# Performance work log

Hardware: AMD Instinct MI355X
Metric: run time of the kernel (lower is better)

Reference implementation:

```python
import jax, jax.numpy as jnp
import numpy as np


def setup_inputs() -> dict:
    key = jax.random.key(0)
    k1, k2, k3 = jax.random.split(key, 3)
    B, D, T, DEPTH = 16384, 512, 64, 6
    x = jax.random.normal(k1, (B, D), dtype=jnp.float32)
    # per-tree learned params, stacked over the tree axis (num_trees)
    feature_selectors = jax.random.normal(k2, (T, DEPTH, D), dtype=jnp.float32)
    thresholds = jnp.zeros((T, DEPTH), dtype=jnp.float32)
    leaf_weights = jax.random.normal(k3, (T, 2 ** DEPTH, 1), dtype=jnp.float32)
    return {"x": x, "feature_selectors": feature_selectors,
            "thresholds": thresholds, "leaf_weights": leaf_weights}


def reference(x, feature_selectors, thresholds, leaf_weights):
    # x: [B, D]; feature_selectors: [T, depth, D]; thresholds: [T, depth]
    # leaf_weights: [T, 2^depth, 1]
    B = x.shape[0]
    T, depth, _ = feature_selectors.shape
    # all trees' split logits in one GEMM: [B, T, depth]
    logits = jnp.einsum('bi,tdi->btd', x, feature_selectors) - thresholds
    probs = jax.nn.sigmoid(logits)
    # probs_stack[..., 0] = p, probs_stack[..., 1] = 1 - p  -> [B, T, depth, 2]
    probs_stack = jnp.stack([probs, 1.0 - probs], axis=-1)
    # build leaf probabilities via repeated outer products over the depth axis
    leaf = probs_stack[:, :, 0]  # [B, T, 2]
    for d in range(1, depth):
        # [B, T, 2^d, 1] * [B, T, 1, 2] -> [B, T, 2^(d+1)]
        leaf = (leaf[..., :, None] * probs_stack[:, :, d][:, :, None, :]).reshape(B, T, -1)
    # per-tree leaf_probs @ weights, summed over trees -> [B, 1]
    out = jnp.einsum('btl,tlo->bo', leaf, leaf_weights)
    return out
```

## Files before the change

### kernel.cpp

```cpp
#include <hip/hip_runtime.h>


#define DD     512
#define NCOL   384
#define PKELT  (NCOL * DD)
#define XSTR   522
#define PRSTR  388

typedef __bf16 bf16_t;
typedef __bf16 bf16x8 __attribute__((ext_vector_type(8)));
typedef __bf16 bf16x4 __attribute__((ext_vector_type(4)));
typedef float  f32x4  __attribute__((ext_vector_type(4)));

static __device__ __forceinline__ float b2f(unsigned int u16) {
  unsigned int t = u16 << 16;
  float f;
  __builtin_memcpy(&f, &t, 4);
  return f;
}

__global__ __launch_bounds__(256) void node_pack(const float* __restrict__ fsel,
                                                 bf16_t* __restrict__ pk)
{
  int tid  = blockIdx.x * 256 + threadIdx.x;
  int lane = tid & 63;
  int ksg  = (tid >> 6) & 15;
  int cf   = tid >> 10;
  int col  = cf * 16 + (lane & 15);
  int k    = ksg * 32 + (lane >> 4) * 8;
  float4 f0 = *reinterpret_cast<const float4*>(fsel + (size_t)col * DD + k);
  float4 f1 = *reinterpret_cast<const float4*>(fsel + (size_t)col * DD + k + 4);
  bf16x8 v;
  v[0] = (bf16_t)f0.x; v[1] = (bf16_t)f0.y; v[2] = (bf16_t)f0.z; v[3] = (bf16_t)f0.w;
  v[4] = (bf16_t)f1.x; v[5] = (bf16_t)f1.y; v[6] = (bf16_t)f1.z; v[7] = (bf16_t)f1.w;
  #pragma unroll
  for (int c = 0; c < 8; ++c)
    *reinterpret_cast<bf16x8*>(pk + (size_t)c * PKELT + (size_t)tid * 8) = v;
}

__global__ __launch_bounds__(512, 2) void node_fused(
    const float*  __restrict__ x,
    const bf16_t* __restrict__ pk,
    const float*  __restrict__ thr,
    const float*  __restrict__ lw,
    float*        __restrict__ out)
{
  __shared__ bf16_t xs[64 * XSTR];
  __shared__ bf16_t pr[64 * PRSTR];

  const int tid  = threadIdx.x;
  const int lane = tid & 63;
  const int wv   = tid >> 6;
  const int rowblk = blockIdx.x * 64;
  const int c   = lane & 15;
  const int kg  = lane >> 4;

  const float* xr0 = x + (size_t)(rowblk + (tid >> 4)) * DD + ((tid & 15) << 2);
  const float* xr1 = xr0 + (size_t)32 * DD;
  bf16_t* xw0 = &xs[(tid >> 4) * XSTR + ((tid & 15) << 2)];
  bf16_t* xw1 = &xs[((tid >> 4) + 32) * XSTR + ((tid & 15) << 2)];

  float th[3];
  #pragma unroll
  for (int f = 0; f < 3; ++f) th[f] = thr[wv * 48 + f * 16 + c];

  float4 stg[2][2];

  #define ISSUE(n, buf)                                                         \
    do {                                                                        \
      int off_ = (n) * 64;                                                      \
      asm volatile("" : "+v"(off_));                                            \
      stg[buf][0] = *reinterpret_cast<const float4*>(xr0 + off_);               \
      stg[buf][1] = *reinterpret_cast<const float4*>(xr1 + off_);               \
    } while (0)

  #define WRITE(n, buf)                                                         \
    do {                                                                        \
      bf16x4 v0_, v1_;                                                          \
      v0_[0]=(bf16_t)stg[buf][0].x; v0_[1]=(bf16_t)stg[buf][0].y;               \
      v0_[2]=(bf16_t)stg[buf][0].z; v0_[3]=(bf16_t)stg[buf][0].w;               \
      v1_[0]=(bf16_t)stg[buf][1].x; v1_[1]=(bf16_t)stg[buf][1].y;               \
      v1_[2]=(bf16_t)stg[buf][1].z; v1_[3]=(bf16_t)stg[buf][1].w;               \
      *reinterpret_cast<bf16x4*>(xw0 + (n) * 64) = v0_;                         \
      *reinterpret_cast<bf16x4*>(xw1 + (n) * 64) = v1_;                         \
    } while (0)

  #define LOAD_BH(B_, n)                                                        \
    do {                                                                        \
      const bf16_t* q_ = pk + (size_t)(blockIdx.x & 7) * PKELT +                \
                         (size_t)lane * 8 + (size_t)(n) * 1024 +                \
                         (size_t)wv * 3 * 8192;                                 \
      asm volatile("" : "+v"(q_));                                              \
      _Pragma("unroll")                                                         \
      for (int f_ = 0; f_ < 3; ++f_)                                            \
        _Pragma("unroll")                                                       \
        for (int ks_ = 0; ks_ < 2; ++ks_)                                       \
          B_[f_][ks_] = *reinterpret_cast<const bf16x8*>(q_ + f_ * 8192 + ks_ * 512); \
    } while (0)

  bf16x8 bhA[3][2], bhB[3][2];

  ISSUE(0, 0);
  LOAD_BH(bhA, 0);
  LOAD_BH(bhB, 1);
  ISSUE(1, 1);
  WRITE(0, 0);
  ISSUE(2, 0);
  asm volatile("s_waitcnt lgkmcnt(0)" ::: "memory");
  __builtin_amdgcn_s_barrier();

  f32x4 acc[4][3];
  #pragma unroll
  for (int t = 0; t < 4; ++t)
    #pragma unroll
    for (int f = 0; f < 3; ++f) acc[t][f] = (f32x4){0.f, 0.f, 0.f, 0.f};

  #define CHUNK(ch, CUR)                                                        \
    do {                                                                        \
      __builtin_amdgcn_s_setprio(1);                                            \
      _Pragma("unroll")                                                         \
      for (int t = 0; t < 4; ++t) {                                             \
        _Pragma("unroll")                                                       \
        for (int ks = 0; ks < 2; ++ks) {                                        \
          bf16x8 a = *reinterpret_cast<const bf16x8*>(                          \
              &xs[(t * 16 + c) * XSTR + (ch) * 64 + ks * 32 + kg * 8]);         \
          acc[t][0] = __builtin_amdgcn_mfma_f32_16x16x32_bf16(a, CUR[0][ks], acc[t][0], 0, 0, 0); \
          acc[t][1] = __builtin_amdgcn_mfma_f32_16x16x32_bf16(a, CUR[1][ks], acc[t][1], 0, 0, 0); \
          acc[t][2] = __builtin_amdgcn_mfma_f32_16x16x32_bf16(a, CUR[2][ks], acc[t][2], 0, 0, 0); \
        }                                                                       \
      }                                                                         \
      __builtin_amdgcn_s_setprio(0);                                            \
      if ((ch) + 2 < 8) LOAD_BH(CUR, (ch) + 2);                                 \
      if ((ch) < 7) {                                                           \
        WRITE((ch) + 1, ((ch) + 1) & 1);                                        \
        if ((ch) < 5) ISSUE((ch) + 3, ((ch) + 1) & 1);                          \
        asm volatile("s_waitcnt lgkmcnt(0)" ::: "memory");                      \
        __builtin_amdgcn_s_barrier();                                           \
      }                                                                         \
    } while (0)

  CHUNK(0, bhA);
  CHUNK(1, bhB);
  CHUNK(2, bhA);
  CHUNK(3, bhB);
  CHUNK(4, bhA);
  CHUNK(5, bhB);
  CHUNK(6, bhA);
  CHUNK(7, bhB);
  #undef CHUNK
  #undef ISSUE
  #undef WRITE
  #undef LOAD_BH

  #pragma unroll
  for (int t = 0; t < 4; ++t) {
    #pragma unroll
    for (int f = 0; f < 3; ++f) {
      const int col = wv * 48 + f * 16 + c;
      #pragma unroll
      for (int r = 0; r < 4; ++r) {
        const int row = t * 16 + kg * 4 + r;
        float z = acc[t][f][r] - th[f];
        float p = 1.0f / (1.0f + __expf(-z));
        pr[row * PRSTR + col] = (bf16_t)p;
      }
    }
  }
  asm volatile("s_waitcnt lgkmcnt(0)" ::: "memory");
  __builtin_amdgcn_s_barrier();

  float p0v[8], hv0[8], hv1[8];
  #pragma unroll
  for (int half = 0; half < 2; ++half) {
    float wch[32];
    #pragma unroll
    for (int j = 0; j < 8; ++j) {
      float4 f4 = *reinterpret_cast<const float4*>(lw + (size_t)lane * 64 + half * 32 + j * 4);
      wch[4*j] = f4.x; wch[4*j+1] = f4.y; wch[4*j+2] = f4.z; wch[4*j+3] = f4.w;
    }
    #pragma unroll
    for (int rr = 0; rr < 8; ++rr) {
      const int row = wv * 8 + rr;
      const unsigned int* prow =
          reinterpret_cast<const unsigned int*>(&pr[row * PRSTR]) + lane * 3;
      unsigned int d0 = prow[0], d1 = prow[1], d2 = prow[2];
      float p1 = b2f(d0 >> 16);
      float p2 = b2f(d1 & 0xffffu), p3 = b2f(d1 >> 16);
      float p4 = b2f(d2 & 0xffffu), p5 = b2f(d2 >> 16);
      if (half == 0) p0v[rr] = b2f(d0 & 0xffffu);

      float v[16];
      #pragma unroll
      for (int j = 0; j < 16; ++j) v[j] = fmaf(p5, wch[2*j] - wch[2*j+1], wch[2*j+1]);
      #pragma unroll
      for (int j = 0; j < 8;  ++j) v[j] = fmaf(p4, v[2*j] - v[2*j+1], v[2*j+1]);
      #pragma unroll
      for (int j = 0; j < 4;  ++j) v[j] = fmaf(p3, v[2*j] - v[2*j+1], v[2*j+1]);
      #pragma unroll
      for (int j = 0; j < 2;  ++j) v[j] = fmaf(p2, v[2*j] - v[2*j+1], v[2*j+1]);
      float s = fmaf(p1, v[0] - v[1], v[1]);
      if (half == 0) hv0[rr] = s; else hv1[rr] = s;
    }
  }

  float tvv[8];
  #pragma unroll
  for (int rr = 0; rr < 8; ++rr)
    tvv[rr] = fmaf(p0v[rr], hv0[rr] - hv1[rr], hv1[rr]);

  #pragma unroll
  for (int off = 32; off; off >>= 1) {
    #pragma unroll
    for (int rr = 0; rr < 8; ++rr) tvv[rr] += __shfl_xor(tvv[rr], off, 64);
  }
  if (lane == 0) {
    #pragma unroll
    for (int rr = 0; rr < 8; ++rr) out[rowblk + wv * 8 + rr] = tvv[rr];
  }
}

extern "C" void kernel_launch(void* const* d_in, const int* in_sizes, int n_in,
                              void* d_out, int out_size, void* d_ws, size_t ws_size,
                              hipStream_t stream) {
  const float* x    = (const float*)d_in[0];
  const float* fsel = (const float*)d_in[1];
  const float* thr  = (const float*)d_in[2];
  const float* lw   = (const float*)d_in[3];
  float* out = (float*)d_out;

  bf16_t* pk = (bf16_t*)d_ws;

  const int B = in_sizes[0] / DD;

  node_pack<<<dim3(96), dim3(256), 0, stream>>>(fsel, pk);
  node_fused<<<dim3(B / 64), dim3(512), 0, stream>>>(x, pk, thr, lw, out);
}
```

Measured before the change: 28.27 us.

## Halve rows per block, prefetch all x chunks up front, raise occupancy

Each block now handles 32 rows instead of 64, so the grid doubles, LDS use per block halves, and launch bounds ask for 4 blocks per CU. All eight x chunks for a thread are loaded into registers at the start instead of through a rolling two-buffer pipeline, and the MFMA priority boosts are dropped. The aim is more resident waves to hide memory latency. In exchange each block reuses its feature-selector (B) fragments over half as many rows, so B traffic from L2 doubles, and more registers are held for x staging.

```diff
diff --git a/kernel.cpp b/kernel.cpp
--- a/kernel.cpp
+++ b/kernel.cpp
@@ -38,51 +38,45 @@
     *reinterpret_cast<bf16x8*>(pk + (size_t)c * PKELT + (size_t)tid * 8) = v;
 }
 
-__global__ __launch_bounds__(512, 2) void node_fused(
+__global__ __launch_bounds__(512, 4) void node_fused(
     const float*  __restrict__ x,
     const bf16_t* __restrict__ pk,
     const float*  __restrict__ thr,
     const float*  __restrict__ lw,
     float*        __restrict__ out)
 {
-  __shared__ bf16_t xs[64 * XSTR];
-  __shared__ bf16_t pr[64 * PRSTR];
+  __shared__ bf16_t xs[32 * XSTR];
+  __shared__ bf16_t pr[32 * PRSTR];
 
   const int tid  = threadIdx.x;
   const int lane = tid & 63;
   const int wv   = tid >> 6;
-  const int rowblk = blockIdx.x * 64;
+  const int rowblk = blockIdx.x * 32;
   const int c   = lane & 15;
   const int kg  = lane >> 4;
 
-  const float* xr0 = x + (size_t)(rowblk + (tid >> 4)) * DD + ((tid & 15) << 2);
-  const float* xr1 = xr0 + (size_t)32 * DD;
-  bf16_t* xw0 = &xs[(tid >> 4) * XSTR + ((tid & 15) << 2)];
-  bf16_t* xw1 = &xs[((tid >> 4) + 32) * XSTR + ((tid & 15) << 2)];
+  const float* xr = x + (size_t)(rowblk + (tid >> 4)) * DD + ((tid & 15) << 2);
+  bf16_t* xw = &xs[(tid >> 4) * XSTR + ((tid & 15) << 2)];
 
   float th[3];
   #pragma unroll
   for (int f = 0; f < 3; ++f) th[f] = thr[wv * 48 + f * 16 + c];
 
-  float4 stg[2][2];
-
-  #define ISSUE(n, buf)                                                         \
+  float4 st[8];
+
+  #define ISSUE(n)                                                              \
     do {                                                                        \
       int off_ = (n) * 64;                                                      \
       asm volatile("" : "+v"(off_));                                            \
-      stg[buf][0] = *reinterpret_cast<const float4*>(xr0 + off_);               \
-      stg[buf][1] = *reinterpret_cast<const float4*>(xr1 + off_);               \
-    } while (0)
-
-  #define WRITE(n, buf)                                                         \
-    do {                                                                        \
-      bf16x4 v0_, v1_;                                                          \
-      v0_[0]=(bf16_t)stg[buf][0].x; v0_[1]=(bf16_t)stg[buf][0].y;               \
-      v0_[2]=(bf16_t)stg[buf][0].z; v0_[3]=(bf16_t)stg[buf][0].w;               \
-      v1_[0]=(bf16_t)stg[buf][1].x; v1_[1]=(bf16_t)stg[buf][1].y;               \
-      v1_[2]=(bf16_t)stg[buf][1].z; v1_[3]=(bf16_t)stg[buf][1].w;               \
-      *reinterpret_cast<bf16x4*>(xw0 + (n) * 64) = v0_;                         \
-      *reinterpret_cast<bf16x4*>(xw1 + (n) * 64) = v1_;                         \
+      st[n] = *reinterpret_cast<const float4*>(xr + off_);                      \
+    } while (0)
+
+  #define WRITE(n)                                                              \
+    do {                                                                        \
+      bf16x4 v_;                                                                \
+      v_[0]=(bf16_t)st[n].x; v_[1]=(bf16_t)st[n].y;                             \
+      v_[2]=(bf16_t)st[n].z; v_[3]=(bf16_t)st[n].w;                             \
+      *reinterpret_cast<bf16x4*>(xw + (n) * 64) = v_;                           \
     } while (0)
 
   #define LOAD_BH(B_, n)                                                        \
@@ -100,40 +94,36 @@
 
   bf16x8 bhA[3][2], bhB[3][2];
 
-  ISSUE(0, 0);
+  ISSUE(0);
   LOAD_BH(bhA, 0);
+  ISSUE(1); ISSUE(2); ISSUE(3); ISSUE(4); ISSUE(5); ISSUE(6); ISSUE(7);
   LOAD_BH(bhB, 1);
-  ISSUE(1, 1);
-  WRITE(0, 0);
-  ISSUE(2, 0);
+  WRITE(0);
   asm volatile("s_waitcnt lgkmcnt(0)" ::: "memory");
   __builtin_amdgcn_s_barrier();
 
-  f32x4 acc[4][3];
-  #pragma unroll
-  for (int t = 0; t < 4; ++t)
-    #pragma unroll
-    for (int f = 0; f < 3; ++f) acc[t][f] = (f32x4){0.f, 0.f, 0.f, 0.f};
+  f32x4 acc[2][3];
+  #pragma unroll
+  for (int rf = 0; rf < 2; ++rf)
+    #pragma unroll
+    for (int f = 0; f < 3; ++f) acc[rf][f] = (f32x4){0.f, 0.f, 0.f, 0.f};
 
   #define CHUNK(ch, CUR)                                                        \
     do {                                                                        \
-      __builtin_amdgcn_s_setprio(1);                                            \
       _Pragma("unroll")                                                         \
-      for (int t = 0; t < 4; ++t) {                                             \
+      for (int rf = 0; rf < 2; ++rf) {                                          \
         _Pragma("unroll")                                                       \
         for (int ks = 0; ks < 2; ++ks) {                                        \
           bf16x8 a = *reinterpret_cast<const bf16x8*>(                          \
-              &xs[(t * 16 + c) * XSTR + (ch) * 64 + ks * 32 + kg * 8]);         \
-          acc[t][0] = __builtin_amdgcn_mfma_f32_16x16x32_bf16(a, CUR[0][ks], acc[t][0], 0, 0, 0); \
-          acc[t][1] = __builtin_amdgcn_mfma_f32_16x16x32_bf16(a, CUR[1][ks], acc[t][1], 0, 0, 0); \
-          acc[t][2] = __builtin_amdgcn_mfma_f32_16x16x32_bf16(a, CUR[2][ks], acc[t][2], 0, 0, 0); \
+              &xs[(rf * 16 + c) * XSTR + (ch) * 64 + ks * 32 + kg * 8]);        \
+          acc[rf][0] = __builtin_amdgcn_mfma_f32_16x16x32_bf16(a, CUR[0][ks], acc[rf][0], 0, 0, 0); \
+          acc[rf][1] = __builtin_amdgcn_mfma_f32_16x16x32_bf16(a, CUR[1][ks], acc[rf][1], 0, 0, 0); \
+          acc[rf][2] = __builtin_amdgcn_mfma_f32_16x16x32_bf16(a, CUR[2][ks], acc[rf][2], 0, 0, 0); \
         }                                                                       \
       }                                                                         \
-      __builtin_amdgcn_s_setprio(0);                                            \
       if ((ch) + 2 < 8) LOAD_BH(CUR, (ch) + 2);                                 \
       if ((ch) < 7) {                                                           \
-        WRITE((ch) + 1, ((ch) + 1) & 1);                                        \
-        if ((ch) < 5) ISSUE((ch) + 3, ((ch) + 1) & 1);                          \
+        WRITE((ch) + 1);                                                        \
         asm volatile("s_waitcnt lgkmcnt(0)" ::: "memory");                      \
         __builtin_amdgcn_s_barrier();                                           \
       }                                                                         \
@@ -153,14 +143,14 @@
   #undef LOAD_BH
 
   #pragma unroll
-  for (int t = 0; t < 4; ++t) {
+  for (int rf = 0; rf < 2; ++rf) {
     #pragma unroll
     for (int f = 0; f < 3; ++f) {
       const int col = wv * 48 + f * 16 + c;
       #pragma unroll
       for (int r = 0; r < 4; ++r) {
-        const int row = t * 16 + kg * 4 + r;
-        float z = acc[t][f][r] - th[f];
+        const int row = rf * 16 + kg * 4 + r;
+        float z = acc[rf][f][r] - th[f];
         float p = 1.0f / (1.0f + __expf(-z));
         pr[row * PRSTR + col] = (bf16_t)p;
       }
@@ -169,7 +159,7 @@
   asm volatile("s_waitcnt lgkmcnt(0)" ::: "memory");
   __builtin_amdgcn_s_barrier();
 
-  float p0v[8], hv0[8], hv1[8];
+  float p0v[4], hv0[4], hv1[4];
   #pragma unroll
   for (int half = 0; half < 2; ++half) {
     float wch[32];
@@ -179,8 +169,8 @@
       wch[4*j] = f4.x; wch[4*j+1] = f4.y; wch[4*j+2] = f4.z; wch[4*j+3] = f4.w;
     }
     #pragma unroll
-    for (int rr = 0; rr < 8; ++rr) {
-      const int row = wv * 8 + rr;
+    for (int rr = 0; rr < 4; ++rr) {
+      const int row = wv * 4 + rr;
       const unsigned int* prow =
           reinterpret_cast<const unsigned int*>(&pr[row * PRSTR]) + lane * 3;
       unsigned int d0 = prow[0], d1 = prow[1], d2 = prow[2];
@@ -203,19 +193,19 @@
     }
   }
 
-  float tvv[8];
-  #pragma unroll
-  for (int rr = 0; rr < 8; ++rr)
+  float tvv[4];
+  #pragma unroll
+  for (int rr = 0; rr < 4; ++rr)
     tvv[rr] = fmaf(p0v[rr], hv0[rr] - hv1[rr], hv1[rr]);
 
   #pragma unroll
   for (int off = 32; off; off >>= 1) {
     #pragma unroll
-    for (int rr = 0; rr < 8; ++rr) tvv[rr] += __shfl_xor(tvv[rr], off, 64);
+    for (int rr = 0; rr < 4; ++rr) tvv[rr] += __shfl_xor(tvv[rr], off, 64);
   }
   if (lane == 0) {
     #pragma unroll
-    for (int rr = 0; rr < 8; ++rr) out[rowblk + wv * 8 + rr] = tvv[rr];
+    for (int rr = 0; rr < 4; ++rr) out[rowblk + wv * 4 + rr] = tvv[rr];
   }
 }
 
@@ -233,5 +223,5 @@
   const int B = in_sizes[0] / DD;
 
   node_pack<<<dim3(96), dim3(256), 0, stream>>>(fsel, pk);
-  node_fused<<<dim3(B / 64), dim3(512), 0, stream>>>(x, pk, thr, lw, out);
-}
+  node_fused<<<dim3(B / 32), dim3(512), 0, stream>>>(x, pk, thr, lw, out);
+}
```

Result: slower. 37.02 us (+31.0%).

## Pre-convert x to bf16 in prep kernel and load tiles via global_load_lds

Applied to the files above, without the earlier changes.

Moves the fp32-to-bf16 conversion of x out of the fused GEMM kernel into an extended prep kernel that writes a bf16 copy to workspace. The fused kernel then loads its whole 64x512 x tile into LDS at once with direct global-to-LDS loads and a single barrier, which removes the per-chunk staging, write and barrier pipeline. It also switches the sigmoid to exp2/rcp intrinsics and drops the setprio hints. The cost is an extra full round trip of x through global memory (fp32 read, bf16 write, bf16 read) and the loss of load/compute overlap inside the fused kernel.

```diff
diff --git a/kernel.cpp b/kernel.cpp
--- a/kernel.cpp
+++ b/kernel.cpp
@@ -4,12 +4,11 @@
 #define DD     512
 #define NCOL   384
 #define PKELT  (NCOL * DD)
-#define XSTR   522
+#define XSTR   520
 #define PRSTR  388
 
 typedef __bf16 bf16_t;
 typedef __bf16 bf16x8 __attribute__((ext_vector_type(8)));
-typedef __bf16 bf16x4 __attribute__((ext_vector_type(4)));
 typedef float  f32x4  __attribute__((ext_vector_type(4)));
 
 static __device__ __forceinline__ float b2f(unsigned int u16) {
@@ -19,27 +18,45 @@
   return f;
 }
 
-__global__ __launch_bounds__(256) void node_pack(const float* __restrict__ fsel,
-                                                 bf16_t* __restrict__ pk)
+static __device__ __forceinline__ float fast_sigmoid(float z) {
+  float e = __builtin_amdgcn_exp2f(z * -1.44269504f);
+  return __builtin_amdgcn_rcpf(1.0f + e);
+}
+
+__global__ __launch_bounds__(256) void node_prep(const float* __restrict__ fsel,
+                                                 const float* __restrict__ x,
+                                                 bf16_t* __restrict__ pk,
+                                                 bf16_t* __restrict__ xbf)
 {
-  int tid  = blockIdx.x * 256 + threadIdx.x;
-  int lane = tid & 63;
-  int ksg  = (tid >> 6) & 15;
-  int cf   = tid >> 10;
-  int col  = cf * 16 + (lane & 15);
-  int k    = ksg * 32 + (lane >> 4) * 8;
-  float4 f0 = *reinterpret_cast<const float4*>(fsel + (size_t)col * DD + k);
-  float4 f1 = *reinterpret_cast<const float4*>(fsel + (size_t)col * DD + k + 4);
-  bf16x8 v;
-  v[0] = (bf16_t)f0.x; v[1] = (bf16_t)f0.y; v[2] = (bf16_t)f0.z; v[3] = (bf16_t)f0.w;
-  v[4] = (bf16_t)f1.x; v[5] = (bf16_t)f1.y; v[6] = (bf16_t)f1.z; v[7] = (bf16_t)f1.w;
-  #pragma unroll
-  for (int c = 0; c < 8; ++c)
-    *reinterpret_cast<bf16x8*>(pk + (size_t)c * PKELT + (size_t)tid * 8) = v;
+  if (blockIdx.x < 96) {
+    int tid  = blockIdx.x * 256 + threadIdx.x;
+    int lane = tid & 63;
+    int ksg  = (tid >> 6) & 15;
+    int cf   = tid >> 10;
+    int col  = cf * 16 + (lane & 15);
+    int k    = ksg * 32 + (lane >> 4) * 8;
+    float4 f0 = *reinterpret_cast<const float4*>(fsel + (size_t)col * DD + k);
+    float4 f1 = *reinterpret_cast<const float4*>(fsel + (size_t)col * DD + k + 4);
+    bf16x8 v;
+    v[0] = (bf16_t)f0.x; v[1] = (bf16_t)f0.y; v[2] = (bf16_t)f0.z; v[3] = (bf16_t)f0.w;
+    v[4] = (bf16_t)f1.x; v[5] = (bf16_t)f1.y; v[6] = (bf16_t)f1.z; v[7] = (bf16_t)f1.w;
+    #pragma unroll
+    for (int c = 0; c < 8; ++c)
+      *reinterpret_cast<bf16x8*>(pk + (size_t)c * PKELT + (size_t)tid * 8) = v;
+  } else {
+    size_t idx = (size_t)(blockIdx.x - 96) * 256 + threadIdx.x;
+    size_t e   = idx * 8;
+    float4 f0 = *reinterpret_cast<const float4*>(x + e);
+    float4 f1 = *reinterpret_cast<const float4*>(x + e + 4);
+    bf16x8 v;
+    v[0] = (bf16_t)f0.x; v[1] = (bf16_t)f0.y; v[2] = (bf16_t)f0.z; v[3] = (bf16_t)f0.w;
+    v[4] = (bf16_t)f1.x; v[5] = (bf16_t)f1.y; v[6] = (bf16_t)f1.z; v[7] = (bf16_t)f1.w;
+    *reinterpret_cast<bf16x8*>(xbf + e) = v;
+  }
 }
 
 __global__ __launch_bounds__(512, 2) void node_fused(
-    const float*  __restrict__ x,
+    const bf16_t* __restrict__ xbf,
     const bf16_t* __restrict__ pk,
     const float*  __restrict__ thr,
     const float*  __restrict__ lw,
@@ -55,36 +72,22 @@
   const int c   = lane & 15;
   const int kg  = lane >> 4;
 
-  const float* xr0 = x + (size_t)(rowblk + (tid >> 4)) * DD + ((tid & 15) << 2);
-  const float* xr1 = xr0 + (size_t)32 * DD;
-  bf16_t* xw0 = &xs[(tid >> 4) * XSTR + ((tid & 15) << 2)];
-  bf16_t* xw1 = &xs[((tid >> 4) + 32) * XSTR + ((tid & 15) << 2)];
-
   float th[3];
   #pragma unroll
   for (int f = 0; f < 3; ++f) th[f] = thr[wv * 48 + f * 16 + c];
 
-  float4 stg[2][2];
-
-  #define ISSUE(n, buf)                                                         \
-    do {                                                                        \
-      int off_ = (n) * 64;                                                      \
-      asm volatile("" : "+v"(off_));                                            \
-      stg[buf][0] = *reinterpret_cast<const float4*>(xr0 + off_);               \
-      stg[buf][1] = *reinterpret_cast<const float4*>(xr1 + off_);               \
-    } while (0)
-
-  #define WRITE(n, buf)                                                         \
-    do {                                                                        \
-      bf16x4 v0_, v1_;                                                          \
-      v0_[0]=(bf16_t)stg[buf][0].x; v0_[1]=(bf16_t)stg[buf][0].y;               \
-      v0_[2]=(bf16_t)stg[buf][0].z; v0_[3]=(bf16_t)stg[buf][0].w;               \
-      v1_[0]=(bf16_t)stg[buf][1].x; v1_[1]=(bf16_t)stg[buf][1].y;               \
-      v1_[2]=(bf16_t)stg[buf][1].z; v1_[3]=(bf16_t)stg[buf][1].w;               \
-      *reinterpret_cast<bf16x4*>(xw0 + (n) * 64) = v0_;                         \
-      *reinterpret_cast<bf16x4*>(xw1 + (n) * 64) = v1_;                         \
-    } while (0)
-
+  #pragma unroll
+  for (int i = 0; i < 8; ++i) {
+    const int row = wv * 8 + i;
+    __builtin_amdgcn_global_load_lds(
+        (const __attribute__((address_space(1))) unsigned int*)(const void*)
+            (xbf + (size_t)(rowblk + row) * DD + lane * 8),
+        (__attribute__((address_space(3))) unsigned int*)(void*)
+            (&xs[row * XSTR]),
+        16, 0, 0);
+  }
+
+  bf16x8 bhA[3][2], bhB[3][2];
   #define LOAD_BH(B_, n)                                                        \
     do {                                                                        \
       const bf16_t* q_ = pk + (size_t)(blockIdx.x & 7) * PKELT +                \
@@ -98,16 +101,11 @@
           B_[f_][ks_] = *reinterpret_cast<const bf16x8*>(q_ + f_ * 8192 + ks_ * 512); \
     } while (0)
 
-  bf16x8 bhA[3][2], bhB[3][2];
-
-  ISSUE(0, 0);
+  asm volatile("s_waitcnt vmcnt(0)" ::: "memory");
+  __builtin_amdgcn_s_barrier();
+
   LOAD_BH(bhA, 0);
   LOAD_BH(bhB, 1);
-  ISSUE(1, 1);
-  WRITE(0, 0);
-  ISSUE(2, 0);
-  asm volatile("s_waitcnt lgkmcnt(0)" ::: "memory");
-  __builtin_amdgcn_s_barrier();
 
   f32x4 acc[4][3];
   #pragma unroll
@@ -117,7 +115,6 @@
 
   #define CHUNK(ch, CUR)                                                        \
     do {                                                                        \
-      __builtin_amdgcn_s_setprio(1);                                            \
       _Pragma("unroll")                                                         \
       for (int t = 0; t < 4; ++t) {                                             \
         _Pragma("unroll")                                                       \
@@ -129,14 +126,7 @@
           acc[t][2] = __builtin_amdgcn_mfma_f32_16x16x32_bf16(a, CUR[2][ks], acc[t][2], 0, 0, 0); \
         }                                                                       \
       }                                                                         \
-      __builtin_amdgcn_s_setprio(0);                                            \
       if ((ch) + 2 < 8) LOAD_BH(CUR, (ch) + 2);                                 \
-      if ((ch) < 7) {                                                           \
-        WRITE((ch) + 1, ((ch) + 1) & 1);                                        \
-        if ((ch) < 5) ISSUE((ch) + 3, ((ch) + 1) & 1);                          \
-        asm volatile("s_waitcnt lgkmcnt(0)" ::: "memory");                      \
-        __builtin_amdgcn_s_barrier();                                           \
-      }                                                                         \
     } while (0)
 
   CHUNK(0, bhA);
@@ -148,8 +138,6 @@
   CHUNK(6, bhA);
   CHUNK(7, bhB);
   #undef CHUNK
-  #undef ISSUE
-  #undef WRITE
   #undef LOAD_BH
 
   #pragma unroll
@@ -160,9 +148,7 @@
       #pragma unroll
       for (int r = 0; r < 4; ++r) {
         const int row = t * 16 + kg * 4 + r;
-        float z = acc[t][f][r] - th[f];
-        float p = 1.0f / (1.0f + __expf(-z));
-        pr[row * PRSTR + col] = (bf16_t)p;
+        pr[row * PRSTR + col] = (bf16_t)fast_sigmoid(acc[t][f][r] - th[f]);
       }
     }
   }
@@ -228,10 +214,12 @@
   const float* lw   = (const float*)d_in[3];
   float* out = (float*)d_out;
 
-  bf16_t* pk = (bf16_t*)d_ws;
+  char* ws = (char*)d_ws;
+  bf16_t* pk  = (bf16_t*)ws;
+  bf16_t* xbf = (bf16_t*)(ws + 8 * 393216);
 
   const int B = in_sizes[0] / DD;
 
-  node_pack<<<dim3(96), dim3(256), 0, stream>>>(fsel, pk);
-  node_fused<<<dim3(B / 64), dim3(512), 0, stream>>>(x, pk, thr, lw, out);
-}
+  node_prep<<<dim3(96 + (B * DD / 8 / 256)), dim3(256), 0, stream>>>(fsel, x, pk, xbf);
+  node_fused<<<dim3(B / 64), dim3(512), 0, stream>>>(xbf, pk, thr, lw, out);
+}
```

After: 30.65 us. 8.4% more time.
